# Performance work log

Measured on AMD Instinct MI355X. Metric: run time of the kernel, lower is better.

The kernel has to match this reference:

```python
import jax, jax.numpy as jnp
import numpy as np

ANG = float(np.deg2rad(20.0))   # rotation/shear range (+/- 20 deg)
MAX_T = 6.0                      # translation range (+/- 6 px)
MAX_Z, MIN_Z = 1.0, 1.0          # zoom fixed to 1 in original


def _affine_params(random, W, H):
    """Vectorized version of the per-sample affine matrix build.
    random: [B] in [0,1). Returns the six entries of the 2x3 matrix, each [B].
    Note: the original uses the SAME random tensor for all params."""
    tx = (MAX_T - (-MAX_T)) * random + (-MAX_T)
    ty = (MAX_T - (-MAX_T)) * random + (-MAX_T)
    r = (ANG - (-ANG)) * random + (-ANG)
    z = (MAX_Z - MIN_Z) * random + MIN_Z
    hx = (ANG - (-ANG)) * random + (-ANG)
    hy = (ANG - (-ANG)) * random + (-ANG)
    a = hx - r
    b = hy + r
    cos_hx, cos_hy = jnp.cos(hx), jnp.cos(hy)
    T11 = z * jnp.cos(a) / cos_hx
    T12 = z * jnp.sin(a) / cos_hx
    T13 = (W * cos_hx - W * z * jnp.cos(a) + 2 * tx * z * jnp.cos(a)
           - H * z * jnp.sin(a) + 2 * ty * z * jnp.sin(a)) / (2 * cos_hx)
    T21 = z * jnp.sin(b) / cos_hy
    T22 = z * jnp.cos(b) / cos_hy
    T23 = (H * cos_hy - W * z * jnp.cos(b) + 2 * ty * z * jnp.cos(b)
           - W * z * jnp.sin(b) + 2 * tx * z * jnp.sin(b)) / (2 * cos_hy)
    return T11, T12, T13, T21, T22, T23


def _bilinear_zeros(img_bhwc, sx, sy):
    """Bilinear sample with zeros padding, pixel coords (align_corners=True).
    img_bhwc: [B,H,W,C]; sx, sy: [B,Ho,Wo] source pixel coordinates."""
    B, H, W, C = img_bhwc.shape
    x0 = jnp.floor(sx)
    y0 = jnp.floor(sy)
    wx = (sx - x0)[..., None]
    wy = (sy - y0)[..., None]
    x0i = x0.astype(jnp.int32)
    y0i = y0.astype(jnp.int32)
    bidx = jnp.arange(B)[:, None, None]

    def gather(xi, yi):
        valid = ((xi >= 0) & (xi < W) & (yi >= 0) & (yi < H))[..., None]
        xc = jnp.clip(xi, 0, W - 1)
        yc = jnp.clip(yi, 0, H - 1)
        v = img_bhwc[bidx, yc, xc]  # [B,Ho,Wo,C]
        return jnp.where(valid, v, 0.0)

    v00 = gather(x0i, y0i)
    v01 = gather(x0i + 1, y0i)
    v10 = gather(x0i, y0i + 1)
    v11 = gather(x0i + 1, y0i + 1)
    return (v00 * (1 - wx) * (1 - wy) + v01 * wx * (1 - wy)
            + v10 * (1 - wx) * wy + v11 * wx * wy)


def reference(img, random):
    # img: [B, C, H, W] (original calls shape[2]=W, shape[3]=H; square images)
    B, C, Hs, Ws = img.shape
    W, H = Hs, Ws  # follow original naming
    T11, T12, T13, T21, T22, T23 = _affine_params(random, W, H)

    # kornia.warp_affine samples src at M^{-1} @ dst (pixel coords).
    det = T11 * T22 - T12 * T21
    i00 = T22 / det
    i01 = -T12 / det
    i10 = -T21 / det
    i11 = T11 / det

    yg, xg = jnp.meshgrid(jnp.arange(Hs, dtype=img.dtype),
                          jnp.arange(Ws, dtype=img.dtype), indexing='ij')
    dx = xg[None] - T13[:, None, None]  # [B,H,W]
    dy = yg[None] - T23[:, None, None]
    sx = i00[:, None, None] * dx + i01[:, None, None] * dy
    sy = i10[:, None, None] * dx + i11[:, None, None] * dy

    out = _bilinear_zeros(jnp.transpose(img, (0, 2, 3, 1)), sx, sy)
    return jnp.transpose(out, (0, 3, 1, 2))  # back to [B,C,H,W]


def setup_inputs() -> dict:
    key = jax.random.key(0)
    k1, k2 = jax.random.split(key)
    img = jax.random.uniform(k1, (128, 3, 256, 256), dtype=jnp.float32)
    random = jax.random.uniform(k2, (128,), dtype=jnp.float32)
    return {"img": img, "random": random}
```

## Files before the change

kernel.cpp:

```cpp
#include <hip/hip_runtime.h>
#include <math.h>


#define AUG_ANG 0.34906585039886590
#define AUG_MAX_T 6.0

#define TW 32
#define TH 128
#define PITCH 36
#define HPITCH (PITCH / 2)
#define MAXROWS 186

__global__ void TCR_params_kernel(const float* __restrict__ rnd,
                                  float* __restrict__ p,
                                  int B, int W, int H) {
    int b = blockIdx.x * blockDim.x + threadIdx.x;
    if (b >= B) return;
    double r01 = (double)rnd[b];
    double tx = 2.0 * AUG_MAX_T * r01 - AUG_MAX_T;
    double ty = tx;
    double r  = 2.0 * AUG_ANG * r01 - AUG_ANG;
    double z  = 1.0;
    double hx = r, hy = r;
    double a  = hx - r;
    double bb = hy + r;
    double cos_hx = cos(hx), cos_hy = cos(hy);
    double ca = cos(a),  sa = sin(a);
    double cb = cos(bb), sb = sin(bb);
    double T11 = z * ca / cos_hx;
    double T12 = z * sa / cos_hx;
    double T13 = ((double)W * cos_hx - (double)W * z * ca + 2.0 * tx * z * ca
                  - (double)H * z * sa + 2.0 * ty * z * sa) / (2.0 * cos_hx);
    double T21 = z * sb / cos_hy;
    double T22 = z * cb / cos_hy;
    double T23 = ((double)H * cos_hy - (double)W * z * cb + 2.0 * ty * z * cb
                  - (double)W * z * sb + 2.0 * tx * z * sb) / (2.0 * cos_hy);
    double det = T11 * T22 - T12 * T21;
    p[b * 6 + 0] = (float)( T22 / det);
    p[b * 6 + 1] = (float)(-T12 / det);
    p[b * 6 + 2] = (float)(-T21 / det);
    p[b * 6 + 3] = (float)( T11 / det);
    p[b * 6 + 4] = (float)T13;
    p[b * 6 + 5] = (float)T23;
}

__global__ __launch_bounds__(256) void TCR_warp_kernel(
        const float* __restrict__ img, const float* __restrict__ p,
        float* __restrict__ out, int H, int W,
        int tilesX, int nTile, int nT, int useSwz) {
    __shared__ float lds[MAXROWS * PITCH];

    const int tid = (int)threadIdx.x;
    int i = (int)blockIdx.x;
    int b, t;
    if (useSwz) {
        int xcd = i & 7;
        int r   = i >> 3;
        b = xcd + 8 * (r / nT);
        t = r % nT;
    } else {
        b = i / nT;
        t = i % nT;
    }
    const int c  = t / nTile;
    const int tt = t - c * nTile;
    const int tileY = tt / tilesX, tileX = tt - tileY * tilesX;
    const int tx0 = tileX * TW, ty0 = tileY * TH;
    const int tx1 = min(tx0 + TW - 1, W - 1);
    const int ty1 = min(ty0 + TH - 1, H - 1);

    const float i00 = p[b * 6 + 0];
    const float i01 = p[b * 6 + 1];
    const float i10 = p[b * 6 + 2];
    const float i11 = p[b * 6 + 3];
    const float T13 = p[b * 6 + 4];
    const float T23 = p[b * 6 + 5];

    const float cx0 = (float)tx0 - T13, cx1 = (float)tx1 - T13;
    const float cy0 = (float)ty0 - T23, cy1 = (float)ty1 - T23;
    const float sxA = i00 * cx0 + i01 * cy0, sxB = i00 * cx1 + i01 * cy0;
    const float sxC = i00 * cx0 + i01 * cy1, sxD = i00 * cx1 + i01 * cy1;
    const float syA = i10 * cx0 + i11 * cy0, syB = i10 * cx1 + i11 * cy0;
    const float syC = i10 * cx0 + i11 * cy1, syD = i10 * cx1 + i11 * cy1;
    const float sxmin = fminf(fminf(sxA, sxB), fminf(sxC, sxD));
    const float symin = fminf(fminf(syA, syB), fminf(syC, syD));
    const float symax = fmaxf(fmaxf(syA, syB), fmaxf(syC, syD));
    const int xs0 = ((int)floorf(sxmin) - 1) & ~1;
    const int ys0 = (int)floorf(symin) - 1;
    const int ys1 = min((int)floorf(symax) + 2, ys0 + MAXROWS - 1);
    const int hs = ys1 - ys0 + 1;

    const size_t plane = (size_t)H * W;
    const float* pl = img + (size_t)b * 3 * plane + (size_t)c * plane;

    {
        const int nPairs = hs * HPITCH;
        for (int j = tid; j < nPairs; j += 256) {
            const int ry = j / HPITCH;
            const int rp = j - ry * HPITCH;
            const int gy = ys0 + ry;
            const int gx = xs0 + 2 * rp;
            const int gyc = min(max(gy, 0), H - 1);
            const int gxc = min(max(gx, 0), W - 2);
            const float2 f = *(const float2*)&pl[(size_t)gyc * W + gxc];
            const bool my  = (unsigned)gy < (unsigned)H;
            const bool mx0 = (unsigned)gx < (unsigned)W;
            const bool mx1 = (unsigned)(gx + 1) < (unsigned)W;
            float2 v;
            v.x = (my & mx0) ? f.x : 0.0f;
            v.y = (my & mx1) ? f.y : 0.0f;
            *(float2*)&lds[2 * j] = v;
        }
    }
    __syncthreads();

    const int xl = tid & 31;
    const int yl = tid >> 5;
    const int x = tx0 + xl;
    if (x > tx1) return;
    const float dx = (float)x - T13;
    const float sx = i00 * dx;
    float* po = out + (size_t)b * 3 * plane + (size_t)c * plane;

    #pragma unroll
    for (int k = 0; k < TH / 8; ++k) {
        const int y = ty0 + yl + 8 * k;
        if (y > ty1) break;
        const float dy = (float)y - T23;
        const float sxk = sx + i01 * dy;
        const float sy  = i10 * dx + i11 * dy;

        const float x0f = floorf(sxk);
        const float y0f = floorf(sy);
        const float wx = sxk - x0f;
        const float wy = sy - y0f;
        const int x0 = (int)x0f;
        const int y0 = (int)y0f;

        const int iA = (y0 - ys0) * PITCH + (x0 - xs0);
        const float v00 = lds[iA];
        const float v01 = lds[iA + 1];
        const float v10 = lds[iA + PITCH];
        const float v11 = lds[iA + PITCH + 1];

        const float w00 = (1.0f - wx) * (1.0f - wy);
        const float w01 = wx * (1.0f - wy);
        const float w10 = (1.0f - wx) * wy;
        const float w11 = wx * wy;

        const float v = v00 * w00 + v01 * w01 + v10 * w10 + v11 * w11;
        __builtin_nontemporal_store(v, &po[(size_t)y * W + x]);
    }
}

extern "C" void kernel_launch(void* const* d_in, const int* in_sizes, int n_in,
                              void* d_out, int out_size, void* d_ws, size_t ws_size,
                              hipStream_t stream) {
    const float* img = (const float*)d_in[0];
    const float* rnd = (const float*)d_in[1];
    float* out = (float*)d_out;
    float* params = (float*)d_ws;

    const int B = in_sizes[1];
    const int C = 3;
    const int total = in_sizes[0];
    const int HW = total / (B * C);
    int W = 256;
    while (W * W > HW) W >>= 1;
    const int H = HW / W;

    TCR_params_kernel<<<(B + 127) / 128, 128, 0, stream>>>(rnd, params, B, W, H);

    const int tilesX = (W + TW - 1) / TW;
    const int tilesY = (H + TH - 1) / TH;
    const int nTile = tilesX * tilesY;
    const int nT = C * nTile;
    const int useSwz = (B % 8 == 0) ? 1 : 0;
    dim3 grid(B * nT);
    TCR_warp_kernel<<<grid, 256, 0, stream>>>(img, params, out, H, W,
                                              tilesX, nTile, nT, useSwz);
}
```

Baseline: 45.54 us.

## Shrink warp tile height, use odd LDS pitch and incremental source coordinates

Halves the output tile height (128 to 64 rows) and shrinks the staged LDS window to match. This gives more, smaller blocks and lower LDS use per block, which may allow higher occupancy. The LDS pitch becomes odd (37) and staging switches from float2 to scalar loads, aiming to reduce bank conflicts on the bilinear gathers at the cost of narrower global loads. The inner loop now advances the source coordinates incrementally and uses the lerp form of bilinear interpolation to cut ALU work. Accumulating coordinates by repeated addition may introduce small rounding differences relative to direct computation.

```diff
diff --git a/kernel.cpp b/kernel.cpp
--- a/kernel.cpp
+++ b/kernel.cpp
@@ -6,10 +6,9 @@
 #define AUG_MAX_T 6.0
 
 #define TW 32
-#define TH 128
-#define PITCH 36
-#define HPITCH (PITCH / 2)
-#define MAXROWS 186
+#define TH 64
+#define PITCH 37
+#define MAXROWS 108
 
 __global__ void TCR_params_kernel(const float* __restrict__ rnd,
                                   float* __restrict__ p,
@@ -48,7 +47,7 @@
         const float* __restrict__ img, const float* __restrict__ p,
         float* __restrict__ out, int H, int W,
         int tilesX, int nTile, int nT, int useSwz) {
-    __shared__ float lds[MAXROWS * PITCH];
+    __shared__ float lds[MAXROWS * PITCH + 2];
 
     const int tid = (int)threadIdx.x;
     int i = (int)blockIdx.x;
@@ -85,7 +84,7 @@
     const float sxmin = fminf(fminf(sxA, sxB), fminf(sxC, sxD));
     const float symin = fminf(fminf(syA, syB), fminf(syC, syD));
     const float symax = fmaxf(fmaxf(syA, syB), fmaxf(syC, syD));
-    const int xs0 = ((int)floorf(sxmin) - 1) & ~1;
+    const int xs0 = (int)floorf(sxmin) - 1;
     const int ys0 = (int)floorf(symin) - 1;
     const int ys1 = min((int)floorf(symax) + 2, ys0 + MAXROWS - 1);
     const int hs = ys1 - ys0 + 1;
@@ -94,22 +93,19 @@
     const float* pl = img + (size_t)b * 3 * plane + (size_t)c * plane;
 
     {
-        const int nPairs = hs * HPITCH;
-        for (int j = tid; j < nPairs; j += 256) {
-            const int ry = j / HPITCH;
-            const int rp = j - ry * HPITCH;
+        const int total = hs * PITCH;
+        for (int j = tid; j < total; j += 256) {
+            const unsigned ju = (unsigned)j;
+            const int ry = (int)(ju / PITCH);
+            const int rx = (int)(ju - (unsigned)ry * PITCH);
             const int gy = ys0 + ry;
-            const int gx = xs0 + 2 * rp;
+            const int gx = xs0 + rx;
             const int gyc = min(max(gy, 0), H - 1);
-            const int gxc = min(max(gx, 0), W - 2);
-            const float2 f = *(const float2*)&pl[(size_t)gyc * W + gxc];
-            const bool my  = (unsigned)gy < (unsigned)H;
-            const bool mx0 = (unsigned)gx < (unsigned)W;
-            const bool mx1 = (unsigned)(gx + 1) < (unsigned)W;
-            float2 v;
-            v.x = (my & mx0) ? f.x : 0.0f;
-            v.y = (my & mx1) ? f.y : 0.0f;
-            *(float2*)&lds[2 * j] = v;
+            const int gxc = min(max(gx, 0), W - 1);
+            const float f = pl[(size_t)gyc * W + gxc];
+            const bool ok = ((unsigned)gx < (unsigned)W) &
+                            ((unsigned)gy < (unsigned)H);
+            lds[j] = ok ? f : 0.0f;
         }
     }
     __syncthreads();
@@ -118,38 +114,42 @@
     const int yl = tid >> 5;
     const int x = tx0 + xl;
     if (x > tx1) return;
-    const float dx = (float)x - T13;
-    const float sx = i00 * dx;
-    float* po = out + (size_t)b * 3 * plane + (size_t)c * plane;
+
+    const float dx  = (float)x - T13;
+    const float dy0 = (float)(ty0 + yl) - T23;
+    float sxl = i00 * dx + i01 * dy0 - (float)xs0;
+    float syl = i10 * dx + i11 * dy0 - (float)ys0;
+    const float dsx = 8.0f * i01;
+    const float dsy = 8.0f * i11;
+
+    float* po = out + (size_t)b * 3 * plane + (size_t)c * plane
+                    + (size_t)(ty0 + yl) * W + x;
 
     #pragma unroll
     for (int k = 0; k < TH / 8; ++k) {
         const int y = ty0 + yl + 8 * k;
         if (y > ty1) break;
-        const float dy = (float)y - T23;
-        const float sxk = sx + i01 * dy;
-        const float sy  = i10 * dx + i11 * dy;
-
-        const float x0f = floorf(sxk);
-        const float y0f = floorf(sy);
-        const float wx = sxk - x0f;
-        const float wy = sy - y0f;
+        const float x0f = floorf(sxl);
+        const float y0f = floorf(syl);
+        const float wx = sxl - x0f;
+        const float wy = syl - y0f;
         const int x0 = (int)x0f;
         const int y0 = (int)y0f;
 
-        const int iA = (y0 - ys0) * PITCH + (x0 - xs0);
+        const int iA = y0 * PITCH + x0;
         const float v00 = lds[iA];
         const float v01 = lds[iA + 1];
         const float v10 = lds[iA + PITCH];
         const float v11 = lds[iA + PITCH + 1];
 
-        const float w00 = (1.0f - wx) * (1.0f - wy);
-        const float w01 = wx * (1.0f - wy);
-        const float w10 = (1.0f - wx) * wy;
-        const float w11 = wx * wy;
+        const float top = v00 + wx * (v01 - v00);
+        const float bot = v10 + wx * (v11 - v10);
+        const float v   = top + wy * (bot - top);
+        __builtin_nontemporal_store(v, po);
 
-        const float v = v00 * w00 + v01 * w01 + v10 * w10 + v11 * w11;
-        __builtin_nontemporal_store(v, &po[(size_t)y * W + x]);
+        po  += 8 * W;
+        sxl += dsx;
+        syl += dsy;
     }
 }
 
```

Result: slower. 55.62 us (+22.1%).
